# Kernel optimization log

Hardware: AMD Instinct MI355X
Metric: run time of the kernel (lower is better)

Reference implementation:

```python
import jax, jax.numpy as jnp
import numpy as np

B, D, T = 32, 384, 4096   # batch, latent_dim, sequence length
K = 256                   # codebook size
BETA = 0.25               # commitment weight


def setup_inputs() -> dict:
    key = jax.random.key(0)
    k1, k2 = jax.random.split(key)
    z = jax.random.normal(k1, (B, D, T), dtype=jnp.float32)
    codebook = jax.random.normal(k2, (K, D), dtype=jnp.float32)
    return {"z": z, "codebook": codebook}


def reference(z, codebook):
    # z: [B, D, T] -> x: [B, T, D]  (the module's permute(0,2,1))
    x = jnp.transpose(z, (0, 2, 1))
    # squared euclidean distance to every code: [B, T, K]
    x2 = jnp.sum(x * x, axis=-1, keepdims=True)            # [B,T,1]
    e2 = jnp.sum(codebook * codebook, axis=-1)             # [K]
    dist = x2 - 2.0 * jnp.einsum('btd,kd->btk', x, codebook) + e2
    indices = jnp.argmin(dist, axis=-1)                    # [B,T] int
    quantize = codebook[indices]                           # gather [B,T,D]
    # commitment loss: beta * mse(stop_grad(quantize), x)
    loss = BETA * jnp.mean(jnp.square(jax.lax.stop_gradient(quantize) - x))
    # straight-through estimator
    quantize = x + jax.lax.stop_gradient(quantize - x)
    # permute back to [B, D, T]
    return jnp.transpose(quantize, (0, 2, 1)), indices, loss
```

## Files before the change

### kernel.cpp

```cpp
#include <hip/hip_runtime.h>

constexpr int BB = 32;
constexpr int DD = 384;
constexpr int TN = 4096;
constexpr int KK = 256;
constexpr float BETA = 0.25f;

constexpr int TT  = 32;
constexpr int DG  = DD / 4;
constexpr int ECH = 2;
constexpr int NCH = DG / ECH;

constexpr size_t QSIZE = (size_t)BB * DD * TN;
constexpr size_t ISIZE = (size_t)BB * TN;

__global__ void e2_kernel(const float* __restrict__ cb, float* __restrict__ e2) {
    int c = threadIdx.x;
    const float4* row = (const float4*)(cb + (size_t)c * DD);
    float s = 0.f;
    #pragma unroll
    for (int g = 0; g < DG; ++g) {
        float4 v = row[g];
        s += v.x * v.x + v.y * v.y + v.z * v.z + v.w * v.w;
    }
    e2[c] = s;
}

__global__ __launch_bounds__(256, 2)
void vq_kernel(const float* __restrict__ z, const float* __restrict__ cb,
               const float* __restrict__ e2g, float* __restrict__ out) {
    __shared__ float4 xs4[DG][TT];
    __shared__ float4 es4[ECH][KK];
    __shared__ float  e2s[KK];
    __shared__ int    idxs[TT];
    __shared__ float  wsum[4];

    const int tid = threadIdx.x;
    const int bid = blockIdx.x;
    const int b   = bid >> 7;
    const int t0  = (bid & 127) * TT;

    const int tx = tid & 31;
    const int ty = tid >> 5;

    e2s[tid] = e2g[tid];

    {
        const float* zb = z + (size_t)b * DD * TN + t0;
        const int tt = tid & 31;
        const int g  = tid >> 5;
        #pragma unroll
        for (int m = 0; m < 12; ++m) {
            int dg = g + 8 * m;
            float4 v;
            v.x = zb[(size_t)(4 * dg + 0) * TN + tt];
            v.y = zb[(size_t)(4 * dg + 1) * TN + tt];
            v.z = zb[(size_t)(4 * dg + 2) * TN + tt];
            v.w = zb[(size_t)(4 * dg + 3) * TN + tt];
            xs4[dg][tt] = v;
        }
    }

    float acc[4][8];
    #pragma unroll
    for (int i = 0; i < 4; ++i)
        #pragma unroll
        for (int j = 0; j < 8; ++j) acc[i][j] = 0.f;

    const float4* cb4 = (const float4*)cb;

    for (int ch = 0; ch < NCH; ++ch) {
        const int dgb = ch * ECH;
        __syncthreads();
        {
            const int c = tid;
            #pragma unroll
            for (int dgl = 0; dgl < ECH; ++dgl)
                es4[dgl][c] = cb4[(size_t)c * DG + dgb + dgl];
        }
        __syncthreads();

        #pragma unroll
        for (int dgl = 0; dgl < ECH; ++dgl) {
            const int dg = dgb + dgl;
            float4 xv[4];
            #pragma unroll
            for (int i = 0; i < 4; ++i) xv[i] = xs4[dg][ty * 4 + i];
            #pragma unroll
            for (int j = 0; j < 8; ++j) {
                float4 ev = es4[dgl][tx + 32 * j];
                #pragma unroll
                for (int i = 0; i < 4; ++i) {
                    acc[i][j] += xv[i].x * ev.x;
                    acc[i][j] += xv[i].y * ev.y;
                    acc[i][j] += xv[i].z * ev.z;
                    acc[i][j] += xv[i].w * ev.w;
                }
            }
        }
    }

    float bv[4]; int bi[4];
    #pragma unroll
    for (int i = 0; i < 4; ++i) { bv[i] = 3.4e38f; bi[i] = 0x7fffffff; }
    #pragma unroll
    for (int j = 0; j < 8; ++j) {
        const int c = tx + 32 * j;
        const float e2c = e2s[c];
        #pragma unroll
        for (int i = 0; i < 4; ++i) {
            float v = e2c - 2.f * acc[i][j];
            if (v < bv[i]) { bv[i] = v; bi[i] = c; }
        }
    }
    #pragma unroll
    for (int m = 16; m >= 1; m >>= 1) {
        #pragma unroll
        for (int i = 0; i < 4; ++i) {
            float ov = __shfl_xor(bv[i], m, 64);
            int   oi = __shfl_xor(bi[i], m, 64);
            if (ov < bv[i] || (ov == bv[i] && oi < bi[i])) { bv[i] = ov; bi[i] = oi; }
        }
    }
    if (tx == 0) {
        #pragma unroll
        for (int i = 0; i < 4; ++i) idxs[ty * 4 + i] = bi[i];
    }
    __syncthreads();

    {
        const int tt = tid & 31;
        const int g  = tid >> 5;
        const int myi = idxs[tt];
        const float4* crow = cb4 + (size_t)myi * DG;
        float* outq = out + (size_t)b * DD * TN + t0;
        float lsum = 0.f;
        #pragma unroll
        for (int m = 0; m < 12; ++m) {
            int dg = g + 8 * m;
            float4 q = crow[dg];
            float4 x = xs4[dg][tt];
            float dx = q.x - x.x, dy = q.y - x.y, dz = q.z - x.z, dw = q.w - x.w;
            lsum += dx * dx + dy * dy + dz * dz + dw * dw;
            outq[(size_t)(4 * dg + 0) * TN + tt] = q.x;
            outq[(size_t)(4 * dg + 1) * TN + tt] = q.y;
            outq[(size_t)(4 * dg + 2) * TN + tt] = q.z;
            outq[(size_t)(4 * dg + 3) * TN + tt] = q.w;
        }
        if (tid < TT)
            out[QSIZE + (size_t)b * TN + t0 + tid] = (float)idxs[tid];

        #pragma unroll
        for (int m = 32; m >= 1; m >>= 1) lsum += __shfl_xor(lsum, m, 64);
        if ((tid & 63) == 0) wsum[tid >> 6] = lsum;
        __syncthreads();
        if (tid == 0) {
            float s = wsum[0] + wsum[1] + wsum[2] + wsum[3];
            atomicAdd(out + QSIZE + ISIZE,
                      s * (BETA / (float)((size_t)BB * DD * TN)));
        }
    }
}

extern "C" void kernel_launch(void* const* d_in, const int* in_sizes, int n_in,
                              void* d_out, int out_size, void* d_ws, size_t ws_size,
                              hipStream_t stream) {
    (void)in_sizes; (void)n_in; (void)out_size; (void)ws_size;
    const float* z  = (const float*)d_in[0];
    const float* cb = (const float*)d_in[1];
    float* out  = (float*)d_out;
    float* e2ws = (float*)d_ws;

    hipMemsetAsync(out + QSIZE + ISIZE, 0, sizeof(float), stream);
    e2_kernel<<<dim3(1), dim3(256), 0, stream>>>(cb, e2ws);
    vq_kernel<<<dim3(BB * (TN / TT)), dim3(256), 0, stream>>>(z, cb, e2ws, out);
}
```

Measured before the change: 724.4 us.

## Stream z tiles through shared memory with register prefetch and larger tiles

After: 942.1 us. 1.3x slower.

```diff
diff --git a/kernel.cpp b/kernel.cpp
--- a/kernel.cpp
+++ b/kernel.cpp
@@ -6,9 +6,9 @@
 constexpr int KK = 256;
 constexpr float BETA = 0.25f;
 
-constexpr int TT  = 32;
+constexpr int TT  = 64;
 constexpr int DG  = DD / 4;
-constexpr int ECH = 2;
+constexpr int ECH = 4;
 constexpr int NCH = DG / ECH;
 
 constexpr size_t QSIZE = (size_t)BB * DD * TN;
@@ -26,71 +26,75 @@
     e2[c] = s;
 }
 
-__global__ __launch_bounds__(256, 2)
+__global__ __launch_bounds__(256, 3)
 void vq_kernel(const float* __restrict__ z, const float* __restrict__ cb,
                const float* __restrict__ e2g, float* __restrict__ out) {
-    __shared__ float4 xs4[DG][TT];
-    __shared__ float4 es4[ECH][KK];
+    __shared__ float4 es4[ECH][KK + 1];
+    __shared__ float4 xs4[ECH][TT];
     __shared__ float  e2s[KK];
     __shared__ int    idxs[TT];
     __shared__ float  wsum[4];
 
     const int tid = threadIdx.x;
     const int bid = blockIdx.x;
-    const int b   = bid >> 7;
-    const int t0  = (bid & 127) * TT;
+    const int b   = bid >> 6;
+    const int t0  = (bid & 63) * TT;
 
     const int tx = tid & 31;
     const int ty = tid >> 5;
 
     e2s[tid] = e2g[tid];
 
-    {
-        const float* zb = z + (size_t)b * DD * TN + t0;
-        const int tt = tid & 31;
-        const int g  = tid >> 5;
-        #pragma unroll
-        for (int m = 0; m < 12; ++m) {
-            int dg = g + 8 * m;
-            float4 v;
-            v.x = zb[(size_t)(4 * dg + 0) * TN + tt];
-            v.y = zb[(size_t)(4 * dg + 1) * TN + tt];
-            v.z = zb[(size_t)(4 * dg + 2) * TN + tt];
-            v.w = zb[(size_t)(4 * dg + 3) * TN + tt];
-            xs4[dg][tt] = v;
-        }
-    }
+    const float*  zb  = z + (size_t)b * DD * TN + t0;
+    const float4* cb4 = (const float4*)cb;
 
-    float acc[4][8];
+    const int ec   = tid >> 2;
+    const int edgl = tid & 3;
+    const int xr   = tid >> 6;
+    const int xtt  = tid & 63;
+
+    float4 epf[4];
+    float  xpf[4];
     #pragma unroll
-    for (int i = 0; i < 4; ++i)
+    for (int s = 0; s < 4; ++s)
+        epf[s] = cb4[(size_t)(ec + 64 * s) * DG + edgl];
+    #pragma unroll
+    for (int c = 0; c < 4; ++c)
+        xpf[c] = zb[(size_t)(4 * xr + c) * TN + xtt];
+
+    float acc[8][8];
+    #pragma unroll
+    for (int i = 0; i < 8; ++i)
         #pragma unroll
         for (int j = 0; j < 8; ++j) acc[i][j] = 0.f;
 
-    const float4* cb4 = (const float4*)cb;
+    for (int ch = 0; ch < NCH; ++ch) {
+        __syncthreads();
+        #pragma unroll
+        for (int s = 0; s < 4; ++s) es4[edgl][ec + 64 * s] = epf[s];
+        xs4[xr][xtt] = make_float4(xpf[0], xpf[1], xpf[2], xpf[3]);
+        __syncthreads();
 
-    for (int ch = 0; ch < NCH; ++ch) {
-        const int dgb = ch * ECH;
-        __syncthreads();
-        {
-            const int c = tid;
+        if (ch + 1 < NCH) {
+            const int dgb = (ch + 1) * ECH;
             #pragma unroll
-            for (int dgl = 0; dgl < ECH; ++dgl)
-                es4[dgl][c] = cb4[(size_t)c * DG + dgb + dgl];
+            for (int s = 0; s < 4; ++s)
+                epf[s] = cb4[(size_t)(ec + 64 * s) * DG + dgb + edgl];
+            #pragma unroll
+            for (int c = 0; c < 4; ++c)
+                xpf[c] = zb[(size_t)(4 * (dgb + xr) + c) * TN + xtt];
         }
-        __syncthreads();
 
         #pragma unroll
         for (int dgl = 0; dgl < ECH; ++dgl) {
-            const int dg = dgb + dgl;
-            float4 xv[4];
+            float4 xv[8];
             #pragma unroll
-            for (int i = 0; i < 4; ++i) xv[i] = xs4[dg][ty * 4 + i];
+            for (int i = 0; i < 8; ++i) xv[i] = xs4[dgl][ty * 8 + i];
             #pragma unroll
             for (int j = 0; j < 8; ++j) {
                 float4 ev = es4[dgl][tx + 32 * j];
                 #pragma unroll
-                for (int i = 0; i < 4; ++i) {
+                for (int i = 0; i < 8; ++i) {
                     acc[i][j] += xv[i].x * ev.x;
                     acc[i][j] += xv[i].y * ev.y;
                     acc[i][j] += xv[i].z * ev.z;
@@ -100,15 +104,15 @@
         }
     }
 
-    float bv[4]; int bi[4];
+    float bv[8]; int bi[8];
     #pragma unroll
-    for (int i = 0; i < 4; ++i) { bv[i] = 3.4e38f; bi[i] = 0x7fffffff; }
+    for (int i = 0; i < 8; ++i) { bv[i] = 3.4e38f; bi[i] = 0x7fffffff; }
     #pragma unroll
     for (int j = 0; j < 8; ++j) {
         const int c = tx + 32 * j;
         const float e2c = e2s[c];
         #pragma unroll
-        for (int i = 0; i < 4; ++i) {
+        for (int i = 0; i < 8; ++i) {
             float v = e2c - 2.f * acc[i][j];
             if (v < bv[i]) { bv[i] = v; bi[i] = c; }
         }
@@ -116,7 +120,7 @@
     #pragma unroll
     for (int m = 16; m >= 1; m >>= 1) {
         #pragma unroll
-        for (int i = 0; i < 4; ++i) {
+        for (int i = 0; i < 8; ++i) {
             float ov = __shfl_xor(bv[i], m, 64);
             int   oi = __shfl_xor(bi[i], m, 64);
             if (ov < bv[i] || (ov == bv[i] && oi < bi[i])) { bv[i] = ov; bi[i] = oi; }
@@ -124,28 +128,29 @@
     }
     if (tx == 0) {
         #pragma unroll
-        for (int i = 0; i < 4; ++i) idxs[ty * 4 + i] = bi[i];
+        for (int i = 0; i < 8; ++i) idxs[ty * 8 + i] = bi[i];
     }
     __syncthreads();
 
     {
-        const int tt = tid & 31;
-        const int g  = tid >> 5;
-        const int myi = idxs[tt];
+        const int myi = idxs[xtt];
         const float4* crow = cb4 + (size_t)myi * DG;
         float* outq = out + (size_t)b * DD * TN + t0;
         float lsum = 0.f;
         #pragma unroll
-        for (int m = 0; m < 12; ++m) {
-            int dg = g + 8 * m;
+        for (int m = 0; m < 24; ++m) {
+            int dg = xr + 4 * m;
             float4 q = crow[dg];
-            float4 x = xs4[dg][tt];
-            float dx = q.x - x.x, dy = q.y - x.y, dz = q.z - x.z, dw = q.w - x.w;
-            lsum += dx * dx + dy * dy + dz * dz + dw * dw;
-            outq[(size_t)(4 * dg + 0) * TN + tt] = q.x;
-            outq[(size_t)(4 * dg + 1) * TN + tt] = q.y;
-            outq[(size_t)(4 * dg + 2) * TN + tt] = q.z;
-            outq[(size_t)(4 * dg + 3) * TN + tt] = q.w;
+            float x0 = zb[(size_t)(4 * dg + 0) * TN + xtt];
+            float x1 = zb[(size_t)(4 * dg + 1) * TN + xtt];
+            float x2 = zb[(size_t)(4 * dg + 2) * TN + xtt];
+            float x3 = zb[(size_t)(4 * dg + 3) * TN + xtt];
+            float d0 = q.x - x0, d1 = q.y - x1, d2 = q.z - x2, d3 = q.w - x3;
+            lsum += d0 * d0 + d1 * d1 + d2 * d2 + d3 * d3;
+            outq[(size_t)(4 * dg + 0) * TN + xtt] = q.x;
+            outq[(size_t)(4 * dg + 1) * TN + xtt] = q.y;
+            outq[(size_t)(4 * dg + 2) * TN + xtt] = q.z;
+            outq[(size_t)(4 * dg + 3) * TN + xtt] = q.w;
         }
         if (tid < TT)
             out[QSIZE + (size_t)b * TN + t0 + tid] = (float)idxs[tid];
```
